# Performance work log

Hardware: AMD Instinct MI355X
Metric: run time of the kernel (lower is better)

## Reference

```python
import jax, jax.numpy as jnp
import numpy as np

EPS = 1e-5
K = 20

def knn_idx(x, k):
    # x: (B, N, C). Torch computes -||xi-xj||^2 and takes topk (largest => nearest).
    xx = jnp.sum(x * x, axis=-1)                      # (B, N)
    inner = jnp.einsum('bnc,bmc->bnm', x, x)          # (B, N, N)
    neg_dist = 2.0 * inner - xx[:, :, None] - xx[:, None, :]
    return jax.lax.top_k(neg_dist, k)[1]              # (B, N, k) int32

def edge_feature(x, k):
    # x: (B, N, C) -> (B, N, k, 2C) = concat(neighbor - center, center)
    B = x.shape[0]
    idx = knn_idx(x, k)
    nb = x[jnp.arange(B)[:, None, None], idx]         # (B, N, k, C) gather
    ctr = jnp.broadcast_to(x[:, :, None, :], nb.shape)
    return jnp.concatenate([nb - ctr, ctr], axis=-1)

def batchnorm(x, gamma, beta, axes):
    # training-mode BN over `axes` (per-channel on last axis)
    m = jnp.mean(x, axis=axes, keepdims=True)
    v = jnp.var(x, axis=axes, keepdims=True)
    return (x - m) * jax.lax.rsqrt(v + EPS) * gamma + beta

def lrelu(x):
    return jnp.where(x >= 0, x, 0.2 * x)

def conv_bn_act(x, w, g, b):
    # 1x1 conv on (B, N, k, Cin) with weight (Cout, Cin), BN over (B, N, k)
    y = jnp.einsum('bnkc,oc->bnko', x, w)
    return lrelu(batchnorm(y, g, b, (0, 1, 2)))


def setup_inputs() -> dict:
    key = jax.random.key(0)
    ks = jax.random.split(key, 16)
    B, N = 4, 4096
    d = {'x': jax.random.normal(ks[0], (B, 3, N), dtype=jnp.float32)}
    d['w1'] = jax.random.normal(ks[1], (64, 6),    dtype=jnp.float32) * 0.1
    d['w2'] = jax.random.normal(ks[2], (64, 64),   dtype=jnp.float32) * 0.1
    d['w3'] = jax.random.normal(ks[3], (64, 128),  dtype=jnp.float32) * 0.1
    d['w4'] = jax.random.normal(ks[4], (64, 64),   dtype=jnp.float32) * 0.1
    d['w5'] = jax.random.normal(ks[5], (64, 128),  dtype=jnp.float32) * 0.1
    d['w6'] = jax.random.normal(ks[6], (1024, 192), dtype=jnp.float32) * 0.05
    d['wl'] = jax.random.normal(ks[7], (512, 1024), dtype=jnp.float32) * 0.05
    for i, c in zip(range(1, 8), [64, 64, 64, 64, 64, 1024, 512]):
        d[f'g{i}'] = jnp.ones((c,), jnp.float32)
        d[f'b{i}'] = jnp.zeros((c,), jnp.float32)
    return d


def reference(x, w1, w2, w3, w4, w5, w6, wl,
              g1, b1, g2, b2, g3, b3, g4, b4, g5, b5, g6, b6, g7, b7):
    p = jnp.transpose(x[:, :3, :], (0, 2, 1))         # (B, N, 3)
    # EdgeConv block 1
    e = edge_feature(p, K)                            # (B, N, k, 6)
    h = conv_bn_act(e, w1, g1, b1)
    h = conv_bn_act(h, w2, g2, b2)
    x1 = jnp.max(h, axis=2)                           # (B, N, 64)
    # EdgeConv block 2
    e = edge_feature(x1, K)                           # (B, N, k, 128)
    h = conv_bn_act(e, w3, g3, b3)
    h = conv_bn_act(h, w4, g4, b4)
    x2 = jnp.max(h, axis=2)
    # EdgeConv block 3
    e = edge_feature(x2, K)
    h = conv_bn_act(e, w5, g5, b5)
    x3 = jnp.max(h, axis=2)
    # point-wise 1x1 conv to 1024 then global max pool
    cat = jnp.concatenate([x1, x2, x3], axis=-1)      # (B, N, 192)
    h = lrelu(batchnorm(jnp.einsum('bnc,oc->bno', cat, w6), g6, b6, (0, 1)))
    g = jnp.max(h, axis=1)                            # (B, 1024)
    out = batchnorm(g @ wl.T, g7, b7, (0,))           # (B, 512)
    return out
```

## Files before the change

### kernel.cpp

```cpp
#include <hip/hip_runtime.h>

static constexpr int PB  = 4;
static constexpr int PN  = 4096;
static constexpr int PK  = 20;
static constexpr int PNT = PB*PN*PK;
#define NEGF (-3.402823466e38f)

__device__ __forceinline__ float lrelu_f(float x){ return x >= 0.f ? x : 0.2f*x; }

#define FMA4C(accv, av, bv) { accv = fmaf((av).x,(bv).x,accv); accv = fmaf((av).y,(bv).y,accv); \
                              accv = fmaf((av).z,(bv).z,accv); accv = fmaf((av).w,(bv).w,accv); }

__global__ __launch_bounds__(256) void k_xx64(const float* __restrict__ f, float* __restrict__ xx){
  int i = blockIdx.x*256 + threadIdx.x;
  if(i >= PB*PN) return;
  const float4* p = (const float4*)(f + (size_t)i*64);
  float t = 0.f;
  #pragma unroll
  for(int c=0;c<16;c++){ float4 v = p[c];
    t = fmaf(v.x,v.x,t); t = fmaf(v.y,v.y,t); t = fmaf(v.z,v.z,t); t = fmaf(v.w,v.w,t); }
  xx[i] = t;
}

__global__ __launch_bounds__(512) void k_knn3(const float* __restrict__ x, int* __restrict__ idxb){
  __shared__ float4 pts[PN];
  int t = threadIdx.x;
  int b = blockIdx.y;
  const float* xb = x + (size_t)b*3*PN;
  for(int i=t;i<PN;i+=512){
    float a0 = xb[i], a1 = xb[PN+i], a2 = xb[2*PN+i];
    float s = a0*a0; s = fmaf(a1,a1,s); s = fmaf(a2,a2,s);
    pts[i] = make_float4(a0,a1,a2,s);
  }
  __syncthreads();
  int lane = t & 63, w = t >> 6;
  int row = blockIdx.x*8 + w;
  float4 pi = pts[row];
  unsigned long long removed = 0ull;

#define KDIST(E) ({ float4 pj_ = pts[lane + ((E)<<6)]; \
    float dt_ = pi.x*pj_.x; dt_ = fmaf(pi.y,pj_.y,dt_); dt_ = fmaf(pi.z,pj_.z,dt_); \
    fmaf(2.f,dt_,-pi.w) - pj_.w; })

  float gv0,gv1,gv2,gv3,gv4,gv5,gv6,gv7;
  int   gi0,gi1,gi2,gi3,gi4,gi5,gi6,gi7;
#define KBUILDG(G) { float gm_=NEGF; int ge_=(G)*8; \
    _Pragma("unroll") for(int e_=(G)*8; e_<(G)*8+8; e_++){ \
      bool ok_ = ((removed >> e_) & 1ull) == 0ull; \
      float d_ = KDIST(e_); \
      bool bt_ = ok_ && (d_ > gm_); gm_ = bt_ ? d_ : gm_; ge_ = bt_ ? e_ : ge_; } \
    gv##G = gm_; gi##G = ge_; }
  KBUILDG(0) KBUILDG(1) KBUILDG(2) KBUILDG(3) KBUILDG(4) KBUILDG(5) KBUILDG(6) KBUILDG(7)

  float lmax; int le;
#define KLBEST { lmax = gv0; le = gi0; \
    if(gv1>lmax){lmax=gv1;le=gi1;} if(gv2>lmax){lmax=gv2;le=gi2;} \
    if(gv3>lmax){lmax=gv3;le=gi3;} if(gv4>lmax){lmax=gv4;le=gi4;} \
    if(gv5>lmax){lmax=gv5;le=gi5;} if(gv6>lmax){lmax=gv6;le=gi6;} \
    if(gv7>lmax){lmax=gv7;le=gi7;} }
  KLBEST

  int myidx = 0;
  for(int k=0;k<PK;k++){
    float bg = lmax; int bj = lane + (le<<6);
    #pragma unroll
    for(int s=1;s<64;s<<=1){
      float og = __shfl_xor(bg, s);
      int   oj = __shfl_xor(bj, s);
      if(og > bg || (og == bg && oj < bj)){ bg = og; bj = oj; }
    }
    if(lane == k) myidx = bj;
    if((bj & 63) == lane){
      int e = bj >> 6;
      removed |= (1ull << e);
      int q = e >> 3;
      if(q==0){ KBUILDG(0) } else if(q==1){ KBUILDG(1) }
      else if(q==2){ KBUILDG(2) } else if(q==3){ KBUILDG(3) }
      else if(q==4){ KBUILDG(4) } else if(q==5){ KBUILDG(5) }
      else if(q==6){ KBUILDG(6) } else { KBUILDG(7) }
      KLBEST
    }
  }
  if(lane < PK) idxb[((size_t)b*PN + row)*PK + lane] = myidx;
#undef KDIST
#undef KBUILDG
#undef KLBEST
}

__global__ __launch_bounds__(256) void k_dist64(const float* __restrict__ Xb, const float* __restrict__ xxb,
                                                float* __restrict__ D){
  extern __shared__ float sm[];
  float* Xi  = sm;
  float* Xj  = Xi + 128*64;
  float* xxi = Xj + 128*64;
  float* xxj = xxi + 128;
  int t = threadIdx.x;
  int p = blockIdx.x;
  int bi = (int)((65.0f - sqrtf(4225.0f - 8.0f*(float)p)) * 0.5f);
  while((bi+1)*32 - ((bi+1)*bi)/2 <= p) bi++;
  while(bi*32 - (bi*(bi-1))/2 > p) bi--;
  int bj = bi + (p - (bi*32 - (bi*(bi-1))/2));
  int i0 = bi*128, j0 = bj*128;
  #pragma unroll
  for(int k=0;k<8;k++){
    int fid = t + k*256; int row = fid>>4, c4 = fid&15;
    ((float4*)Xi)[row*16 + (c4^(row&15))] = ((const float4*)(Xb + (size_t)(i0+row)*64))[c4];
    ((float4*)Xj)[row*16 + (c4^(row&15))] = ((const float4*)(Xb + (size_t)(j0+row)*64))[c4];
  }
  if(t < 128) xxi[t] = xxb[i0+t];
  else        xxj[t-128] = xxb[j0+t-128];
  __syncthreads();
  int prg = t>>4, cq = t&15;
  float acc[8][8];
  #pragma unroll
  for(int pp=0;pp<8;pp++)
    #pragma unroll
    for(int oc=0;oc<8;oc++) acc[pp][oc] = 0.f;
  #pragma unroll 4
  for(int c4=0;c4<16;c4++){
    float4 a[8], bb[8];
    #pragma unroll
    for(int pp=0;pp<8;pp++){ int row = prg*8+pp; a[pp] = ((const float4*)Xi)[row*16 + (c4^(row&15))]; }
    #pragma unroll
    for(int oc=0;oc<8;oc++){ int col = cq+16*oc;  bb[oc] = ((const float4*)Xj)[col*16 + (c4^(col&15))]; }
    #pragma unroll
    for(int pp=0;pp<8;pp++)
      #pragma unroll
      for(int oc=0;oc<8;oc++) FMA4C(acc[pp][oc], a[pp], bb[oc]);
  }
  #pragma unroll
  for(int pp=0;pp<8;pp++){
    int r = prg*8+pp;
    float xi2 = xxi[r];
    float* Drow = D + (size_t)(i0+r)*PN + j0;
    #pragma unroll
    for(int oc=0;oc<8;oc++){
      int c = cq + 16*oc;
      Drow[c] = fmaf(2.f, acc[pp][oc], -xi2) - xxj[c];
    }
  }
  if(bi != bj){
    #pragma unroll
    for(int oc=0;oc<8;oc++){
      int c = cq + 16*oc;
      float xj2 = xxj[c];
      float* Dcol = D + (size_t)(j0+c)*PN + i0 + prg*8;
      float4 t0, t1;
      t0.x = fmaf(2.f, acc[0][oc], -xj2) - xxi[prg*8+0];
      t0.y = fmaf(2.f, acc[1][oc], -xj2) - xxi[prg*8+1];
      t0.z = fmaf(2.f, acc[2][oc], -xj2) - xxi[prg*8+2];
      t0.w = fmaf(2.f, acc[3][oc], -xj2) - xxi[prg*8+3];
      t1.x = fmaf(2.f, acc[4][oc], -xj2) - xxi[prg*8+4];
      t1.y = fmaf(2.f, acc[5][oc], -xj2) - xxi[prg*8+5];
      t1.z = fmaf(2.f, acc[6][oc], -xj2) - xxi[prg*8+6];
      t1.w = fmaf(2.f, acc[7][oc], -xj2) - xxi[prg*8+7];
      ((float4*)Dcol)[0] = t0;
      ((float4*)Dcol)[1] = t1;
    }
  }
}

__global__ __launch_bounds__(256) void k_topk(const float* __restrict__ D, int* __restrict__ idxb){
  int t = threadIdx.x, lane = t & 63, w = t >> 6;
  int row = blockIdx.x*4 + w;
  const float4* rp = (const float4*)(D + (size_t)row*PN + lane*64);
  float v[64];
  #pragma unroll
  for(int c=0;c<16;c++){
    float4 q = rp[c];
    v[4*c+0]=q.x; v[4*c+1]=q.y; v[4*c+2]=q.z; v[4*c+3]=q.w;
  }
  unsigned long long removed = 0ull;
  float gv0,gv1,gv2,gv3,gv4,gv5,gv6,gv7;
  int   gi0,gi1,gi2,gi3,gi4,gi5,gi6,gi7;
#define TBUILDG(G) { float gm_=NEGF; int ge_=(G)*8; \
    _Pragma("unroll") for(int e_=(G)*8; e_<(G)*8+8; e_++){ \
      bool ok_ = ((removed >> e_) & 1ull) == 0ull; \
      bool bt_ = ok_ && (v[e_] > gm_); gm_ = bt_ ? v[e_] : gm_; ge_ = bt_ ? e_ : ge_; } \
    gv##G = gm_; gi##G = ge_; }
  TBUILDG(0) TBUILDG(1) TBUILDG(2) TBUILDG(3) TBUILDG(4) TBUILDG(5) TBUILDG(6) TBUILDG(7)
  float lmax; int li;
#define TLBEST { lmax = gv0; li = gi0; \
    if(gv1>lmax){lmax=gv1;li=gi1;} if(gv2>lmax){lmax=gv2;li=gi2;} \
    if(gv3>lmax){lmax=gv3;li=gi3;} if(gv4>lmax){lmax=gv4;li=gi4;} \
    if(gv5>lmax){lmax=gv5;li=gi5;} if(gv6>lmax){lmax=gv6;li=gi6;} \
    if(gv7>lmax){lmax=gv7;li=gi7;} }
  TLBEST
  int myidx = 0;
  for(int k=0;k<PK;k++){
    float g = lmax;
    #pragma unroll
    for(int s=32;s>=1;s>>=1) g = fmaxf(g, __shfl_xor(g, s));
    unsigned long long mask = __ballot(lmax == g);
    int wl = __ffsll((unsigned long long)mask) - 1;
    int rel = __shfl(li, wl);
    if(lane == k) myidx = wl*64 + rel;
    if(lane == wl){
      removed |= (1ull << rel);
      int q = rel >> 3;
      if(q==0){ TBUILDG(0) } else if(q==1){ TBUILDG(1) }
      else if(q==2){ TBUILDG(2) } else if(q==3){ TBUILDG(3) }
      else if(q==4){ TBUILDG(4) } else if(q==5){ TBUILDG(5) }
      else if(q==6){ TBUILDG(6) } else { TBUILDG(7) }
      TLBEST
    }
  }
  if(lane < PK) idxb[row*PK + lane] = myidx;
#undef TBUILDG
#undef TLBEST
}

__global__ __launch_bounds__(256) void k_nodeUV3(const float* __restrict__ x, const float* __restrict__ w1,
                                                 float* __restrict__ U, float* __restrict__ V){
  __shared__ float ww[384];
  int t = threadIdx.x;
  for(int k=t;k<384;k+=256) ww[k] = w1[k];
  __syncthreads();
  int g = blockIdx.x*256 + t;
  int ng = g >> 6, o = g & 63;
  int b = ng >> 12, n = ng & 4095;
  const float* xb = x + (size_t)b*3*PN;
  float p0 = xb[n], p1 = xb[PN+n], p2 = xb[2*PN+n];
  const float* wr = ww + o*6;
  float u = p0*wr[0]; u = fmaf(p1,wr[1],u); u = fmaf(p2,wr[2],u);
  float vv = p0*(wr[3]-wr[0]); vv = fmaf(p1, wr[4]-wr[1], vv); vv = fmaf(p2, wr[5]-wr[2], vv);
  U[(size_t)ng*64+o] = u;
  V[(size_t)ng*64+o] = vv;
}

__global__ __launch_bounds__(256) void k_nodeUV64(const float* __restrict__ xf, const float* __restrict__ w,
                                                  float* __restrict__ U, float* __restrict__ V){
  __shared__ float xbuf[128*64];
  __shared__ float wbuf[128*64];
  int t = threadIdx.x;
  int r0 = blockIdx.x * 128;
  #pragma unroll
  for(int k=0;k<8;k++){
    int fid = t + k*256; int row = fid>>4, c4 = fid&15;
    ((float4*)xbuf)[row*16 + (c4^(row&15))] = ((const float4*)(xf + (size_t)(r0+row)*64))[c4];
    float4 wv;
    if(row < 64){
      wv = ((const float4*)(w + (size_t)row*128))[c4];
    } else {
      float4 w2v = ((const float4*)(w + (size_t)(row-64)*128 + 64))[c4];
      float4 w1v = ((const float4*)(w + (size_t)(row-64)*128))[c4];
      wv.x = w2v.x-w1v.x; wv.y = w2v.y-w1v.y; wv.z = w2v.z-w1v.z; wv.w = w2v.w-w1v.w;
    }
    ((float4*)wbuf)[row*16 + (c4^(row&15))] = wv;
  }
  __syncthreads();
  int rg = t>>4, cq = t&15;
  float acc[8][8];
  #pragma unroll
  for(int pp=0;pp<8;pp++)
    #pragma unroll
    for(int oc=0;oc<8;oc++) acc[pp][oc] = 0.f;
  #pragma unroll 4
  for(int c4=0;c4<16;c4++){
    float4 a[8], bb[8];
    #pragma unroll
    for(int pp=0;pp<8;pp++){ int row = rg*8+pp; a[pp] = ((const float4*)xbuf)[row*16 + (c4^(row&15))]; }
    #pragma unroll
    for(int oc=0;oc<8;oc++){ int col = cq+16*oc;  bb[oc] = ((const float4*)wbuf)[col*16 + (c4^(col&15))]; }
    #pragma unroll
    for(int pp=0;pp<8;pp++)
      #pragma unroll
      for(int oc=0;oc<8;oc++) FMA4C(acc[pp][oc], a[pp], bb[oc]);
  }
  #pragma unroll
  for(int pp=0;pp<8;pp++){
    int r = r0 + rg*8+pp;
    #pragma unroll
    for(int oc=0;oc<8;oc++){
      int col = cq + 16*oc;
      if(col < 64) U[(size_t)r*64 + col] = acc[pp][oc];
      else         V[(size_t)r*64 + col-64] = acc[pp][oc];
    }
  }
}

__global__ __launch_bounds__(256) void k_statUV(const float* __restrict__ U, const float* __restrict__ V,
                                                const int* __restrict__ idx, float* __restrict__ part){
  __shared__ float ls[512];
  int t = threadIdx.x; int blk = blockIdx.x;
  int ch = t & 63, sub = t >> 6;
  int qbase = blk*640;
  float s = 0.f, qq = 0.f;
  for(int r=sub; r<640; r+=4){
    int q = qbase + r;
    int pt = q/PK;
    int b = pt >> 12;
    int j = idx[q];
    float yv = U[(size_t)(b*PN+j)*64 + ch] + V[(size_t)pt*64 + ch];
    s += yv; qq = fmaf(yv,yv,qq);
  }
  ls[t] = s; ls[256+t] = qq;
  __syncthreads();
  if(t < 64){
    float S = ls[t]+ls[64+t]+ls[128+t]+ls[192+t];
    float Q = ls[256+t]+ls[320+t]+ls[384+t]+ls[448+t];
    part[(size_t)blk*128 + t] = S; part[(size_t)blk*128 + 64 + t] = Q;
  }
}

__global__ __launch_bounds__(256) void k_convAF(const float* __restrict__ U, const float* __restrict__ V,
                                                const int* __restrict__ idx, const float* __restrict__ wg,
                                                const float* __restrict__ sb, float* __restrict__ y){
  __shared__ float hbuf[128*64];
  __shared__ float wbuf[64*64];
  int t = threadIdx.x;
  int q0 = blockIdx.x * 128;
  #pragma unroll
  for(int k=0;k<8;k++){
    int fid = t + k*256; int row = fid>>4, c4 = fid&15;
    int q = q0 + row;
    int pt = q/PK; int b = pt>>12; int j = idx[q];
    float4 uu = ((const float4*)(U + (size_t)(b*PN+j)*64))[c4];
    float4 vv = ((const float4*)(V + (size_t)pt*64))[c4];
    float4 sc = ((const float4*)sb)[c4];
    float4 bi = ((const float4*)(sb+1024))[c4];
    float4 h;
    h.x = lrelu_f(fmaf(uu.x+vv.x, sc.x, bi.x));
    h.y = lrelu_f(fmaf(uu.y+vv.y, sc.y, bi.y));
    h.z = lrelu_f(fmaf(uu.z+vv.z, sc.z, bi.z));
    h.w = lrelu_f(fmaf(uu.w+vv.w, sc.w, bi.w));
    ((float4*)hbuf)[row*16 + (c4 ^ (row&15))] = h;
  }
  #pragma unroll
  for(int k=0;k<4;k++){
    int fid = t + k*256; int row = fid>>4, c4 = fid&15;
    ((float4*)wbuf)[row*16 + (c4 ^ (row&15))] = ((const float4*)(wg + row*64))[c4];
  }
  __syncthreads();
  int prg = t >> 4, cq = t & 15;
  float acc[8][4];
  #pragma unroll
  for(int pp=0;pp<8;pp++)
    #pragma unroll
    for(int oc=0;oc<4;oc++) acc[pp][oc] = 0.f;
  #pragma unroll 4
  for(int c4=0;c4<16;c4++){
    float4 a[8], b4[4];
    #pragma unroll
    for(int pp=0;pp<8;pp++){ int row = prg*8+pp; a[pp] = ((const float4*)hbuf)[row*16 + (c4^(row&15))]; }
    #pragma unroll
    for(int oc=0;oc<4;oc++){ int och = cq + 16*oc; b4[oc] = ((const float4*)wbuf)[och*16 + (c4^(och&15))]; }
    #pragma unroll
    for(int pp=0;pp<8;pp++)
      #pragma unroll
      for(int oc=0;oc<4;oc++) FMA4C(acc[pp][oc], a[pp], b4[oc]);
  }
  #pragma unroll
  for(int pp=0;pp<8;pp++)
    #pragma unroll
    for(int oc=0;oc<4;oc++)
      y[(size_t)(q0 + prg*8+pp)*64 + cq + 16*oc] = acc[pp][oc];
}

__global__ __launch_bounds__(256) void k_red64(const float* __restrict__ y, float* __restrict__ part){
  __shared__ float ls[512];
  int t = threadIdx.x; int blk = blockIdx.x;
  int ch = t & 63, sub = t >> 6;
  const float* base = y + (size_t)blk*640*64;
  float s = 0.f, q = 0.f;
  for(int r=sub; r<640; r+=4){ float v = base[(size_t)r*64 + ch]; s += v; q = fmaf(v,v,q); }
  ls[t] = s; ls[256+t] = q;
  __syncthreads();
  if(t < 64){
    float S = ls[t]+ls[64+t]+ls[128+t]+ls[192+t];
    float Q = ls[256+t]+ls[320+t]+ls[384+t]+ls[448+t];
    part[(size_t)blk*128 + t] = S; part[(size_t)blk*128 + 64 + t] = Q;
  }
}

__global__ __launch_bounds__(256) void k_red1024(const float* __restrict__ y6, float* __restrict__ part){
  int t = threadIdx.x; int blk = blockIdx.x;
  const float4* base = (const float4*)(y6 + (size_t)blk*128*1024);
  float4 s = make_float4(0,0,0,0), q = make_float4(0,0,0,0);
  for(int r=0;r<128;r++){
    float4 v = base[r*256 + t];
    s.x += v.x; s.y += v.y; s.z += v.z; s.w += v.w;
    q.x = fmaf(v.x,v.x,q.x); q.y = fmaf(v.y,v.y,q.y); q.z = fmaf(v.z,v.z,q.z); q.w = fmaf(v.w,v.w,q.w);
  }
  ((float4*)(part + (size_t)blk*2048))[t] = s;
  ((float4*)(part + (size_t)blk*2048 + 1024))[t] = q;
}

__global__ __launch_bounds__(256) void k_fin(const float* __restrict__ part, int nparts, int chn, float cnt,
                                             const float* __restrict__ gamma, const float* __restrict__ beta,
                                             float* __restrict__ sb){
  __shared__ float ls[512];
  int t = threadIdx.x;
  int chl = t & 15, sub = t >> 4;
  int ch = blockIdx.x*16 + chl;
  float S = 0.f, Q = 0.f;
  for(int p=sub; p<nparts; p+=16){
    S += part[(size_t)p*2*chn + ch];
    Q += part[(size_t)p*2*chn + chn + ch];
  }
  ls[t] = S; ls[256+t] = Q;
  __syncthreads();
  if(t < 16){
    float Sa = 0.f, Qa = 0.f;
    #pragma unroll
    for(int s=0;s<16;s++){ Sa += ls[s*16+t]; Qa += ls[256+s*16+t]; }
    int c = blockIdx.x*16 + t;
    float m  = Sa/cnt;
    float vr = Qa/cnt - m*m;
    float sc = gamma[c] * rsqrtf(vr + 1e-5f);
    sb[c] = sc; sb[1024+c] = beta[c] - m*sc;
  }
}

__global__ __launch_bounds__(256) void k_finish(const float* __restrict__ y, const float* __restrict__ sb,
                                                float* __restrict__ xo){
  int t = threadIdx.x;
  int pt = blockIdx.x*16 + (t>>4), c4 = t&15;
  const float4* base = (const float4*)(y + (size_t)pt*20*64);
  float4 sc = ((const float4*)sb)[c4];
  float4 bi = ((const float4*)(sb+1024))[c4];
  float4 m = make_float4(NEGF,NEGF,NEGF,NEGF);
  #pragma unroll 4
  for(int k=0;k<20;k++){
    float4 v = base[k*16 + c4];
    v.x = lrelu_f(fmaf(v.x, sc.x, bi.x)); v.y = lrelu_f(fmaf(v.y, sc.y, bi.y));
    v.z = lrelu_f(fmaf(v.z, sc.z, bi.z)); v.w = lrelu_f(fmaf(v.w, sc.w, bi.w));
    m.x = fmaxf(m.x,v.x); m.y = fmaxf(m.y,v.y); m.z = fmaxf(m.z,v.z); m.w = fmaxf(m.w,v.w);
  }
  ((float4*)(xo + (size_t)pt*64))[c4] = m;
}

__global__ __launch_bounds__(256) void k_finishUV(const float* __restrict__ U, const float* __restrict__ V,
                                                  const int* __restrict__ idx, const float* __restrict__ sb,
                                                  float* __restrict__ xo){
  int t = threadIdx.x;
  int pt = blockIdx.x*16 + (t>>4), c4 = t&15;
  int b = pt >> 12;
  float4 sc = ((const float4*)sb)[c4];
  float4 bi = ((const float4*)(sb+1024))[c4];
  float4 vv = ((const float4*)(V + (size_t)pt*64))[c4];
  float4 m = make_float4(NEGF,NEGF,NEGF,NEGF);
  const int* ip = idx + (size_t)pt*PK;
  #pragma unroll 4
  for(int k=0;k<PK;k++){
    int j = ip[k];
    float4 uu = ((const float4*)(U + (size_t)(b*PN+j)*64))[c4];
    float4 v;
    v.x = lrelu_f(fmaf(uu.x+vv.x, sc.x, bi.x)); v.y = lrelu_f(fmaf(uu.y+vv.y, sc.y, bi.y));
    v.z = lrelu_f(fmaf(uu.z+vv.z, sc.z, bi.z)); v.w = lrelu_f(fmaf(uu.w+vv.w, sc.w, bi.w));
    m.x = fmaxf(m.x,v.x); m.y = fmaxf(m.y,v.y); m.z = fmaxf(m.z,v.z); m.w = fmaxf(m.w,v.w);
  }
  ((float4*)(xo + (size_t)pt*64))[c4] = m;
}

__global__ __launch_bounds__(256) void k_gemm6(const float* __restrict__ x1, const float* __restrict__ x2,
                                               const float* __restrict__ x3, const float* __restrict__ w6,
                                               float* __restrict__ y6){
  __shared__ float cb[128*64];
  __shared__ float wb[64*64];
  int t = threadIdx.x;
  int rb = blockIdx.x >> 4;
  int ob = blockIdx.x & 15;
  size_t r0 = (size_t)rb*128; int o0 = ob*64;
  int prg = t >> 4, cq = t & 15;
  float acc[8][4];
  #pragma unroll
  for(int pp=0;pp<8;pp++)
    #pragma unroll
    for(int oc=0;oc<4;oc++) acc[pp][oc] = 0.f;
  const float* srcs[3] = {x1, x2, x3};
  for(int ph=0; ph<3; ph++){
    __syncthreads();
    const float* src = srcs[ph];
    #pragma unroll
    for(int k=0;k<8;k++){
      int fid = t + k*256; int row = fid>>4, c4 = fid&15;
      ((float4*)cb)[row*16 + (c4^(row&15))] = ((const float4*)(src + (r0+row)*64))[c4];
    }
    #pragma unroll
    for(int k=0;k<4;k++){
      int fid = t + k*256; int row = fid>>4, c4 = fid&15;
      ((float4*)wb)[row*16 + (c4^(row&15))] = ((const float4*)(w6 + (size_t)(o0+row)*192 + ph*64))[c4];
    }
    __syncthreads();
    #pragma unroll 4
    for(int c4=0;c4<16;c4++){
      float4 a[8], b4[4];
      #pragma unroll
      for(int pp=0;pp<8;pp++){ int row = prg*8+pp; a[pp] = ((const float4*)cb)[row*16 + (c4^(row&15))]; }
      #pragma unroll
      for(int oc=0;oc<4;oc++){ int och = cq + 16*oc; b4[oc] = ((const float4*)wb)[och*16 + (c4^(och&15))]; }
      #pragma unroll
      for(int pp=0;pp<8;pp++)
        #pragma unroll
        for(int oc=0;oc<4;oc++) FMA4C(acc[pp][oc], a[pp], b4[oc]);
    }
  }
  #pragma unroll
  for(int pp=0;pp<8;pp++)
    #pragma unroll
    for(int oc=0;oc<4;oc++)
      y6[(r0 + prg*8+pp)*1024 + o0 + cq + 16*oc] = acc[pp][oc];
}

__global__ __launch_bounds__(256) void k_gmax(const float* __restrict__ y6, const float* __restrict__ sb,
                                              float* __restrict__ gpart){
  int t = threadIdx.x; int blk = blockIdx.x;
  const float4* base = (const float4*)(y6 + (size_t)blk*256*1024);
  float4 sc = ((const float4*)sb)[t];
  float4 bi = ((const float4*)(sb+1024))[t];
  float4 m = make_float4(NEGF,NEGF,NEGF,NEGF);
  for(int r=0;r<256;r++){
    float4 v = base[r*256 + t];
    v.x = lrelu_f(fmaf(v.x, sc.x, bi.x)); v.y = lrelu_f(fmaf(v.y, sc.y, bi.y));
    v.z = lrelu_f(fmaf(v.z, sc.z, bi.z)); v.w = lrelu_f(fmaf(v.w, sc.w, bi.w));
    m.x = fmaxf(m.x,v.x); m.y = fmaxf(m.y,v.y); m.z = fmaxf(m.z,v.z); m.w = fmaxf(m.w,v.w);
  }
  ((float4*)(gpart + (size_t)blk*1024))[t] = m;
}

__global__ __launch_bounds__(256) void k_gmaxfin(const float* __restrict__ gpart, float* __restrict__ g){
  int b = blockIdx.x, t = threadIdx.x;
  float4 m = make_float4(NEGF,NEGF,NEGF,NEGF);
  for(int c=0;c<16;c++){
    float4 v = ((const float4*)(gpart + ((size_t)b*16 + c)*1024))[t];
    m.x = fmaxf(m.x,v.x); m.y = fmaxf(m.y,v.y); m.z = fmaxf(m.z,v.z); m.w = fmaxf(m.w,v.w);
  }
  ((float4*)(g + (size_t)b*1024))[t] = m;
}

__global__ __launch_bounds__(256) void k_final(const float* __restrict__ g, const float* __restrict__ wl,
                                               const float* __restrict__ g7, const float* __restrict__ b7,
                                               float* __restrict__ out){
  int gt = blockIdx.x*256 + threadIdx.x;
  int o = gt >> 2, b = gt & 3;
  const float4* gb = (const float4*)(g + (size_t)b*1024);
  const float4* wr = (const float4*)(wl + (size_t)o*1024);
  float acc = 0.f;
  #pragma unroll 4
  for(int c=0;c<256;c++){
    float4 a = gb[c], w = wr[c];
    acc = fmaf(a.x,w.x,acc); acc = fmaf(a.y,w.y,acc);
    acc = fmaf(a.z,w.z,acc); acc = fmaf(a.w,w.w,acc);
  }
  float s = acc + __shfl_xor(acc, 1);
  s = s + __shfl_xor(s, 2);
  float m = s * 0.25f;
  float d = acc - m;
  float vv = d*d;
  float v2 = vv + __shfl_xor(vv, 1);
  v2 = v2 + __shfl_xor(v2, 2);
  float var = v2 * 0.25f;
  out[b*512 + o] = d * rsqrtf(var + 1e-5f) * g7[o] + b7[o];
}

extern "C" void kernel_launch(void* const* d_in, const int* in_sizes, int n_in,
                              void* d_out, int out_size, void* d_ws, size_t ws_size,
                              hipStream_t stream){
  const float* x  = (const float*)d_in[0];
  const float* w1 = (const float*)d_in[1];
  const float* w2 = (const float*)d_in[2];
  const float* w3 = (const float*)d_in[3];
  const float* w4 = (const float*)d_in[4];
  const float* w5 = (const float*)d_in[5];
  const float* w6 = (const float*)d_in[6];
  const float* wl = (const float*)d_in[7];
  const float* g1 = (const float*)d_in[8];  const float* b1 = (const float*)d_in[9];
  const float* g2 = (const float*)d_in[10]; const float* b2 = (const float*)d_in[11];
  const float* g3 = (const float*)d_in[12]; const float* b3 = (const float*)d_in[13];
  const float* g4 = (const float*)d_in[14]; const float* b4 = (const float*)d_in[15];
  const float* g5 = (const float*)d_in[16]; const float* b5 = (const float*)d_in[17];
  const float* g6 = (const float*)d_in[18]; const float* b6 = (const float*)d_in[19];
  const float* g7 = (const float*)d_in[20]; const float* b7 = (const float*)d_in[21];
  float* out = (float*)d_out;

  float* ws    = (float*)d_ws;
  float* xx    = ws;
  int*   idx   = (int*)(ws + 16384);
  float* y     = ws + 344064;
  float* Dbuf  = y;
  float* x1    = ws + 21315584;
  float* x2    = x1 + 1048576;
  float* x3    = x2 + 1048576;
  float* part  = x3 + 1048576;
  float* sb    = part + 262144;
  float* gpart = sb + 2048;
  float* g     = gpart + 65536;
  float* U     = g + 4096;
  float* V     = U + 1048576;

  hipFuncSetAttribute(reinterpret_cast<const void*>(&k_dist64),
                      hipFuncAttributeMaxDynamicSharedMemorySize, 66560);

  k_knn3<<<dim3(512,4),512,0,stream>>>(x, idx);
  k_nodeUV3<<<4096,256,0,stream>>>(x, w1, U, V);
  k_statUV<<<512,256,0,stream>>>(U, V, idx, part);
  k_fin<<<4,256,0,stream>>>(part, 512, 64, (float)PNT, g1, b1, sb);
  k_convAF<<<2560,256,0,stream>>>(U, V, idx, w2, sb, y);
  k_red64<<<512,256,0,stream>>>(y, part);
  k_fin<<<4,256,0,stream>>>(part, 512, 64, (float)PNT, g2, b2, sb);
  k_finish<<<1024,256,0,stream>>>(y, sb, x1);

  k_xx64<<<64,256,0,stream>>>(x1, xx);
  for(int b=0;b<PB;b++){
    k_dist64<<<528,256,66560,stream>>>(x1 + (size_t)b*PN*64, xx + b*PN, Dbuf);
    k_topk<<<1024,256,0,stream>>>(Dbuf, idx + (size_t)b*PN*PK);
  }
  k_nodeUV64<<<128,256,0,stream>>>(x1, w3, U, V);
  k_statUV<<<512,256,0,stream>>>(U, V, idx, part);
  k_fin<<<4,256,0,stream>>>(part, 512, 64, (float)PNT, g3, b3, sb);
  k_convAF<<<2560,256,0,stream>>>(U, V, idx, w4, sb, y);
  k_red64<<<512,256,0,stream>>>(y, part);
  k_fin<<<4,256,0,stream>>>(part, 512, 64, (float)PNT, g4, b4, sb);
  k_finish<<<1024,256,0,stream>>>(y, sb, x2);

  k_xx64<<<64,256,0,stream>>>(x2, xx);
  for(int b=0;b<PB;b++){
    k_dist64<<<528,256,66560,stream>>>(x2 + (size_t)b*PN*64, xx + b*PN, Dbuf);
    k_topk<<<1024,256,0,stream>>>(Dbuf, idx + (size_t)b*PN*PK);
  }
  k_nodeUV64<<<128,256,0,stream>>>(x2, w5, U, V);
  k_statUV<<<512,256,0,stream>>>(U, V, idx, part);
  k_fin<<<4,256,0,stream>>>(part, 512, 64, (float)PNT, g5, b5, sb);
  k_finishUV<<<1024,256,0,stream>>>(U, V, idx, sb, x3);

  k_gemm6<<<2048,256,0,stream>>>(x1, x2, x3, w6, y);
  k_red1024<<<128,256,0,stream>>>(y, part);
  k_fin<<<64,256,0,stream>>>(part, 128, 1024, 16384.f, g6, b6, sb);
  k_gmax<<<64,256,0,stream>>>(y, sb, gpart);
  k_gmaxfin<<<4,256,0,stream>>>(gpart, g);
  k_final<<<8,256,0,stream>>>(g, wl, g7, b7, out);
}
```

Baseline: 1.341 ms.

## Fuse BN stats into conv, fuse xx into finish, shrink dist smem, pack knn keys

Several independent changes. Per-channel BN partial sums are moved into the convAF epilogue, removing the k_red64 pass over y, and the squared norms are computed inside k_finish, removing k_xx64. k_dist64 stages its operands in two 32-channel halves of static shared memory for higher occupancy. The knn3 argmax reduction packs value and index into one 64-bit key, topk poisons removed entries instead of tracking a removed mask, and statUV is vectorised to float4. The risks are extra barriers in dist64 and a larger partial buffer that k_fin must reduce.

```diff
diff --git a/kernel.cpp b/kernel.cpp
--- a/kernel.cpp
+++ b/kernel.cpp
@@ -8,19 +8,14 @@
 
 __device__ __forceinline__ float lrelu_f(float x){ return x >= 0.f ? x : 0.2f*x; }
 
+__device__ __forceinline__ unsigned int ordf(float v){
+  unsigned int u = __float_as_uint(v);
+  unsigned int mask = ((unsigned int)(((int)u) >> 31)) | 0x80000000u;
+  return u ^ mask;
+}
+
 #define FMA4C(accv, av, bv) { accv = fmaf((av).x,(bv).x,accv); accv = fmaf((av).y,(bv).y,accv); \
                               accv = fmaf((av).z,(bv).z,accv); accv = fmaf((av).w,(bv).w,accv); }
-
-__global__ __launch_bounds__(256) void k_xx64(const float* __restrict__ f, float* __restrict__ xx){
-  int i = blockIdx.x*256 + threadIdx.x;
-  if(i >= PB*PN) return;
-  const float4* p = (const float4*)(f + (size_t)i*64);
-  float t = 0.f;
-  #pragma unroll
-  for(int c=0;c<16;c++){ float4 v = p[c];
-    t = fmaf(v.x,v.x,t); t = fmaf(v.y,v.y,t); t = fmaf(v.z,v.z,t); t = fmaf(v.w,v.w,t); }
-  xx[i] = t;
-}
 
 __global__ __launch_bounds__(512) void k_knn3(const float* __restrict__ x, int* __restrict__ idxb){
   __shared__ float4 pts[PN];
@@ -62,16 +57,17 @@
 
   int myidx = 0;
   for(int k=0;k<PK;k++){
-    float bg = lmax; int bj = lane + (le<<6);
+    unsigned long long key = ((unsigned long long)ordf(lmax) << 32) |
+                             (unsigned int)(~(lane + (le<<6)));
     #pragma unroll
     for(int s=1;s<64;s<<=1){
-      float og = __shfl_xor(bg, s);
-      int   oj = __shfl_xor(bj, s);
-      if(og > bg || (og == bg && oj < bj)){ bg = og; bj = oj; }
-    }
-    if(lane == k) myidx = bj;
-    if((bj & 63) == lane){
-      int e = bj >> 6;
+      unsigned long long o = __shfl_xor(key, s);
+      if(o > key) key = o;
+    }
+    int jw = (int)(~((unsigned int)key));
+    if(lane == k) myidx = jw;
+    if((jw & 63) == lane){
+      int e = jw >> 6;
       removed |= (1ull << e);
       int q = e >> 3;
       if(q==0){ KBUILDG(0) } else if(q==1){ KBUILDG(1) }
@@ -89,11 +85,9 @@
 
 __global__ __launch_bounds__(256) void k_dist64(const float* __restrict__ Xb, const float* __restrict__ xxb,
                                                 float* __restrict__ D){
-  extern __shared__ float sm[];
-  float* Xi  = sm;
-  float* Xj  = Xi + 128*64;
-  float* xxi = Xj + 128*64;
-  float* xxj = xxi + 128;
+  __shared__ float Xi[128*32];
+  __shared__ float Xj[128*32];
+  __shared__ float xxi[128], xxj[128];
   int t = threadIdx.x;
   int p = blockIdx.x;
   int bi = (int)((65.0f - sqrtf(4225.0f - 8.0f*(float)p)) * 0.5f);
@@ -101,32 +95,38 @@
   while(bi*32 - (bi*(bi-1))/2 > p) bi--;
   int bj = bi + (p - (bi*32 - (bi*(bi-1))/2));
   int i0 = bi*128, j0 = bj*128;
-  #pragma unroll
-  for(int k=0;k<8;k++){
-    int fid = t + k*256; int row = fid>>4, c4 = fid&15;
-    ((float4*)Xi)[row*16 + (c4^(row&15))] = ((const float4*)(Xb + (size_t)(i0+row)*64))[c4];
-    ((float4*)Xj)[row*16 + (c4^(row&15))] = ((const float4*)(Xb + (size_t)(j0+row)*64))[c4];
-  }
-  if(t < 128) xxi[t] = xxb[i0+t];
-  else        xxj[t-128] = xxb[j0+t-128];
-  __syncthreads();
   int prg = t>>4, cq = t&15;
   float acc[8][8];
   #pragma unroll
   for(int pp=0;pp<8;pp++)
     #pragma unroll
     for(int oc=0;oc<8;oc++) acc[pp][oc] = 0.f;
-  #pragma unroll 4
-  for(int c4=0;c4<16;c4++){
-    float4 a[8], bb[8];
-    #pragma unroll
-    for(int pp=0;pp<8;pp++){ int row = prg*8+pp; a[pp] = ((const float4*)Xi)[row*16 + (c4^(row&15))]; }
-    #pragma unroll
-    for(int oc=0;oc<8;oc++){ int col = cq+16*oc;  bb[oc] = ((const float4*)Xj)[col*16 + (c4^(col&15))]; }
-    #pragma unroll
-    for(int pp=0;pp<8;pp++)
-      #pragma unroll
-      for(int oc=0;oc<8;oc++) FMA4C(acc[pp][oc], a[pp], bb[oc]);
+
+  for(int h=0;h<2;h++){
+    if(h) __syncthreads();
+    #pragma unroll
+    for(int k=0;k<4;k++){
+      int fid = t + k*256; int row = fid>>3, c4 = fid&7;
+      ((float4*)Xi)[row*8 + (c4^(row&7))] = ((const float4*)(Xb + (size_t)(i0+row)*64 + h*32))[c4];
+      ((float4*)Xj)[row*8 + (c4^(row&7))] = ((const float4*)(Xb + (size_t)(j0+row)*64 + h*32))[c4];
+    }
+    if(h==0){
+      if(t < 128) xxi[t] = xxb[i0+t];
+      else        xxj[t-128] = xxb[j0+t-128];
+    }
+    __syncthreads();
+    #pragma unroll 4
+    for(int c4=0;c4<8;c4++){
+      float4 a[8], bb[8];
+      #pragma unroll
+      for(int pp=0;pp<8;pp++){ int row = prg*8+pp; a[pp] = ((const float4*)Xi)[row*8 + (c4^(row&7))]; }
+      #pragma unroll
+      for(int oc=0;oc<8;oc++){ int col = cq+16*oc;  bb[oc] = ((const float4*)Xj)[col*8 + (c4^(col&7))]; }
+      #pragma unroll
+      for(int pp=0;pp<8;pp++)
+        #pragma unroll
+        for(int oc=0;oc<8;oc++) FMA4C(acc[pp][oc], a[pp], bb[oc]);
+    }
   }
   #pragma unroll
   for(int pp=0;pp<8;pp++){
@@ -170,14 +170,14 @@
     float4 q = rp[c];
     v[4*c+0]=q.x; v[4*c+1]=q.y; v[4*c+2]=q.z; v[4*c+3]=q.w;
   }
-  unsigned long long removed = 0ull;
   float gv0,gv1,gv2,gv3,gv4,gv5,gv6,gv7;
   int   gi0,gi1,gi2,gi3,gi4,gi5,gi6,gi7;
 #define TBUILDG(G) { float gm_=NEGF; int ge_=(G)*8; \
     _Pragma("unroll") for(int e_=(G)*8; e_<(G)*8+8; e_++){ \
-      bool ok_ = ((removed >> e_) & 1ull) == 0ull; \
-      bool bt_ = ok_ && (v[e_] > gm_); gm_ = bt_ ? v[e_] : gm_; ge_ = bt_ ? e_ : ge_; } \
+      bool bt_ = v[e_] > gm_; gm_ = bt_ ? v[e_] : gm_; ge_ = bt_ ? e_ : ge_; } \
     gv##G = gm_; gi##G = ge_; }
+#define TPOIS(G) { _Pragma("unroll") for(int e_=(G)*8; e_<(G)*8+8; e_++){ \
+      if(e_ == rel) v[e_] = NEGF; } }
   TBUILDG(0) TBUILDG(1) TBUILDG(2) TBUILDG(3) TBUILDG(4) TBUILDG(5) TBUILDG(6) TBUILDG(7)
   float lmax; int li;
 #define TLBEST { lmax = gv0; li = gi0; \
@@ -196,17 +196,17 @@
     int rel = __shfl(li, wl);
     if(lane == k) myidx = wl*64 + rel;
     if(lane == wl){
-      removed |= (1ull << rel);
       int q = rel >> 3;
-      if(q==0){ TBUILDG(0) } else if(q==1){ TBUILDG(1) }
-      else if(q==2){ TBUILDG(2) } else if(q==3){ TBUILDG(3) }
-      else if(q==4){ TBUILDG(4) } else if(q==5){ TBUILDG(5) }
-      else if(q==6){ TBUILDG(6) } else { TBUILDG(7) }
+      if(q==0){ TPOIS(0) TBUILDG(0) } else if(q==1){ TPOIS(1) TBUILDG(1) }
+      else if(q==2){ TPOIS(2) TBUILDG(2) } else if(q==3){ TPOIS(3) TBUILDG(3) }
+      else if(q==4){ TPOIS(4) TBUILDG(4) } else if(q==5){ TPOIS(5) TBUILDG(5) }
+      else if(q==6){ TPOIS(6) TBUILDG(6) } else { TPOIS(7) TBUILDG(7) }
       TLBEST
     }
   }
   if(lane < PK) idxb[row*PK + lane] = myidx;
 #undef TBUILDG
+#undef TPOIS
 #undef TLBEST
 }
 
@@ -281,31 +281,44 @@
 
 __global__ __launch_bounds__(256) void k_statUV(const float* __restrict__ U, const float* __restrict__ V,
                                                 const int* __restrict__ idx, float* __restrict__ part){
-  __shared__ float ls[512];
+  __shared__ float4 sArr[256];
+  __shared__ float4 qArr[256];
   int t = threadIdx.x; int blk = blockIdx.x;
-  int ch = t & 63, sub = t >> 6;
+  int ch4 = t & 15, sub = t >> 4;
   int qbase = blk*640;
-  float s = 0.f, qq = 0.f;
-  for(int r=sub; r<640; r+=4){
+  float4 s = make_float4(0,0,0,0), qq = make_float4(0,0,0,0);
+  for(int r=sub; r<640; r+=16){
     int q = qbase + r;
     int pt = q/PK;
     int b = pt >> 12;
     int j = idx[q];
-    float yv = U[(size_t)(b*PN+j)*64 + ch] + V[(size_t)pt*64 + ch];
-    s += yv; qq = fmaf(yv,yv,qq);
-  }
-  ls[t] = s; ls[256+t] = qq;
-  __syncthreads();
-  if(t < 64){
-    float S = ls[t]+ls[64+t]+ls[128+t]+ls[192+t];
-    float Q = ls[256+t]+ls[320+t]+ls[384+t]+ls[448+t];
-    part[(size_t)blk*128 + t] = S; part[(size_t)blk*128 + 64 + t] = Q;
+    float4 u4 = ((const float4*)(U + (size_t)(b*PN+j)*64))[ch4];
+    float4 v4 = ((const float4*)(V + (size_t)pt*64))[ch4];
+    float4 y4;
+    y4.x = u4.x+v4.x; y4.y = u4.y+v4.y; y4.z = u4.z+v4.z; y4.w = u4.w+v4.w;
+    s.x += y4.x; s.y += y4.y; s.z += y4.z; s.w += y4.w;
+    qq.x = fmaf(y4.x,y4.x,qq.x); qq.y = fmaf(y4.y,y4.y,qq.y);
+    qq.z = fmaf(y4.z,y4.z,qq.z); qq.w = fmaf(y4.w,y4.w,qq.w);
+  }
+  sArr[t] = s; qArr[t] = qq;
+  __syncthreads();
+  if(t < 16){
+    float4 S = make_float4(0,0,0,0), Q = make_float4(0,0,0,0);
+    #pragma unroll
+    for(int g=0;g<16;g++){
+      float4 a = sArr[g*16 + t], b = qArr[g*16 + t];
+      S.x+=a.x; S.y+=a.y; S.z+=a.z; S.w+=a.w;
+      Q.x+=b.x; Q.y+=b.y; Q.z+=b.z; Q.w+=b.w;
+    }
+    ((float4*)(part + (size_t)blk*128))[t] = S;
+    ((float4*)(part + (size_t)blk*128 + 64))[t] = Q;
   }
 }
 
 __global__ __launch_bounds__(256) void k_convAF(const float* __restrict__ U, const float* __restrict__ V,
                                                 const int* __restrict__ idx, const float* __restrict__ wg,
-                                                const float* __restrict__ sb, float* __restrict__ y){
+                                                const float* __restrict__ sb, float* __restrict__ y,
+                                                float* __restrict__ part){
   __shared__ float hbuf[128*64];
   __shared__ float wbuf[64*64];
   int t = threadIdx.x;
@@ -355,21 +368,29 @@
     #pragma unroll
     for(int oc=0;oc<4;oc++)
       y[(size_t)(q0 + prg*8+pp)*64 + cq + 16*oc] = acc[pp][oc];
-}
-
-__global__ __launch_bounds__(256) void k_red64(const float* __restrict__ y, float* __restrict__ part){
-  __shared__ float ls[512];
-  int t = threadIdx.x; int blk = blockIdx.x;
-  int ch = t & 63, sub = t >> 6;
-  const float* base = y + (size_t)blk*640*64;
-  float s = 0.f, q = 0.f;
-  for(int r=sub; r<640; r+=4){ float v = base[(size_t)r*64 + ch]; s += v; q = fmaf(v,v,q); }
-  ls[t] = s; ls[256+t] = q;
+
+  float s_[4], q_[4];
+  #pragma unroll
+  for(int oc=0;oc<4;oc++){
+    float s = 0.f, q = 0.f;
+    #pragma unroll
+    for(int pp=0;pp<8;pp++){ s += acc[pp][oc]; q = fmaf(acc[pp][oc], acc[pp][oc], q); }
+    s_[oc] = s; q_[oc] = q;
+  }
+  __syncthreads();
+  float* ls = wbuf;
+  #pragma unroll
+  for(int oc=0;oc<4;oc++){
+    ls[(cq + 16*oc)*16 + prg]        = s_[oc];
+    ls[2048 + (cq + 16*oc)*16 + prg] = q_[oc];
+  }
   __syncthreads();
   if(t < 64){
-    float S = ls[t]+ls[64+t]+ls[128+t]+ls[192+t];
-    float Q = ls[256+t]+ls[320+t]+ls[384+t]+ls[448+t];
-    part[(size_t)blk*128 + t] = S; part[(size_t)blk*128 + 64 + t] = Q;
+    float S = 0.f, Q = 0.f;
+    #pragma unroll
+    for(int g=0;g<16;g++){ S += ls[t*16+g]; Q += ls[2048 + t*16+g]; }
+    part[(size_t)blockIdx.x*128 + t] = S;
+    part[(size_t)blockIdx.x*128 + 64 + t] = Q;
   }
 }
 
@@ -413,7 +434,8 @@
 }
 
 __global__ __launch_bounds__(256) void k_finish(const float* __restrict__ y, const float* __restrict__ sb,
-                                                float* __restrict__ xo){
+                                                float* __restrict__ xo, float* __restrict__ xxo){
+  __shared__ float ls[256];
   int t = threadIdx.x;
   int pt = blockIdx.x*16 + (t>>4), c4 = t&15;
   const float4* base = (const float4*)(y + (size_t)pt*20*64);
@@ -428,6 +450,15 @@
     m.x = fmaxf(m.x,v.x); m.y = fmaxf(m.y,v.y); m.z = fmaxf(m.z,v.z); m.w = fmaxf(m.w,v.w);
   }
   ((float4*)(xo + (size_t)pt*64))[c4] = m;
+  float ss = m.x*m.x; ss = fmaf(m.y,m.y,ss); ss = fmaf(m.z,m.z,ss); ss = fmaf(m.w,m.w,ss);
+  ls[t] = ss;
+  __syncthreads();
+  if(c4 == 0){
+    float S = 0.f;
+    #pragma unroll
+    for(int c=0;c<16;c++) S += ls[(t & 0xF0) + c];
+    xxo[pt] = S;
+  }
 }
 
 __global__ __launch_bounds__(256) void k_finishUV(const float* __restrict__ U, const float* __restrict__ V,
@@ -583,40 +614,33 @@
   float* x2    = x1 + 1048576;
   float* x3    = x2 + 1048576;
   float* part  = x3 + 1048576;
-  float* sb    = part + 262144;
+  float* sb    = part + 327680;
   float* gpart = sb + 2048;
   float* g     = gpart + 65536;
   float* U     = g + 4096;
   float* V     = U + 1048576;
 
-  hipFuncSetAttribute(reinterpret_cast<const void*>(&k_dist64),
-                      hipFuncAttributeMaxDynamicSharedMemorySize, 66560);
-
   k_knn3<<<dim3(512,4),512,0,stream>>>(x, idx);
   k_nodeUV3<<<4096,256,0,stream>>>(x, w1, U, V);
   k_statUV<<<512,256,0,stream>>>(U, V, idx, part);
   k_fin<<<4,256,0,stream>>>(part, 512, 64, (float)PNT, g1, b1, sb);
-  k_convAF<<<2560,256,0,stream>>>(U, V, idx, w2, sb, y);
-  k_red64<<<512,256,0,stream>>>(y, part);
-  k_fin<<<4,256,0,stream>>>(part, 512, 64, (float)PNT, g2, b2, sb);
-  k_finish<<<1024,256,0,stream>>>(y, sb, x1);
-
-  k_xx64<<<64,256,0,stream>>>(x1, xx);
+  k_convAF<<<2560,256,0,stream>>>(U, V, idx, w2, sb, y, part);
+  k_fin<<<4,256,0,stream>>>(part, 2560, 64, (float)PNT, g2, b2, sb);
+  k_finish<<<1024,256,0,stream>>>(y, sb, x1, xx);
+
   for(int b=0;b<PB;b++){
-    k_dist64<<<528,256,66560,stream>>>(x1 + (size_t)b*PN*64, xx + b*PN, Dbuf);
+    k_dist64<<<528,256,0,stream>>>(x1 + (size_t)b*PN*64, xx + b*PN, Dbuf);
     k_topk<<<1024,256,0,stream>>>(Dbuf, idx + (size_t)b*PN*PK);
   }
   k_nodeUV64<<<128,256,0,stream>>>(x1, w3, U, V);
   k_statUV<<<512,256,0,stream>>>(U, V, idx, part);
   k_fin<<<4,256,0,stream>>>(part, 512, 64, (float)PNT, g3, b3, sb);
-  k_convAF<<<2560,256,0,stream>>>(U, V, idx, w4, sb, y);
-  k_red64<<<512,256,0,stream>>>(y, part);
-  k_fin<<<4,256,0,stream>>>(part, 512, 64, (float)PNT, g4, b4, sb);
-  k_finish<<<1024,256,0,stream>>>(y, sb, x2);
-
-  k_xx64<<<64,256,0,stream>>>(x2, xx);
+  k_convAF<<<2560,256,0,stream>>>(U, V, idx, w4, sb, y, part);
+  k_fin<<<4,256,0,stream>>>(part, 2560, 64, (float)PNT, g4, b4, sb);
+  k_finish<<<1024,256,0,stream>>>(y, sb, x2, xx);
+
   for(int b=0;b<PB;b++){
-    k_dist64<<<528,256,66560,stream>>>(x2 + (size_t)b*PN*64, xx + b*PN, Dbuf);
+    k_dist64<<<528,256,0,stream>>>(x2 + (size_t)b*PN*64, xx + b*PN, Dbuf);
     k_topk<<<1024,256,0,stream>>>(Dbuf, idx + (size_t)b*PN*PK);
   }
   k_nodeUV64<<<128,256,0,stream>>>(x2, w5, U, V);
```

After: 1.254 ms. 1.07x faster.
